# Optimization experiments

Measured on AMD Instinct MI355X. Metric: run time of the kernel, lower is better.

## Reference

```python
import jax, jax.numpy as jnp
import numpy as np

R = 3            # window radius -> (2R+1)^2 = 49 neighbors
N = 128          # grid side, n
K = 131          # 3 + 64 + 64 channels
C = 21           # num_classes
B = 2            # batch
W = (2 * R + 1) ** 2


def setup_inputs() -> dict:
    key = jax.random.key(0)
    k1, k2, k3, k4 = jax.random.split(key, 4)
    return {
        "intergrated": jax.random.normal(k1, (B, K, N, N), jnp.float32),
        "x2": jax.random.normal(k2, (B, C, N * N), jnp.float32),
        "sel_mask": jax.random.randint(k3, (B, N, N), 0, 2).astype(jnp.int32),
        "conv_parameter": jax.random.uniform(k4, (K,), jnp.float32),
    }


def _shifts(x, r):
    """Gather (2r+1)^2 shifted copies: x [..., n, n] -> [..., n, n, W].
    Entry w=(di,dj) holds x[i+di-r, j+dj-r] (zero-padded out of bounds)."""
    n = x.shape[-1]
    pad = [(0, 0)] * (x.ndim - 2) + [(r, r), (r, r)]
    xp = jnp.pad(x, pad)
    cols = [xp[..., di:di + n, dj:dj + n]
            for di in range(2 * r + 1) for dj in range(2 * r + 1)]
    return jnp.stack(cols, axis=-1)


def _rwn_single(feats, x2b, maskb, conv_parameter):
    """feats [K,n,n], x2b [C,n^2], maskb [n,n] int -> y [n^2, C]."""
    n = feats.shape[-1]
    m = maskb.astype(feats.dtype)            # sampled-pixel indicator
    xm = feats * m                            # sparse-sampled features [K,n,n]
    nbr = _shifts(xm, R)                      # [K,n,n,W] neighbor values
    valid = _shifts(jnp.ones((n, n), feats.dtype), R) > 0  # [n,n,W] in-bounds
    # per-channel windowed L1 distance, exp, per-pixel normalization (softmax
    # of +distance over the valid window, as in the original code)
    d = jnp.abs(xm[..., None] - nbr)          # [K,n,n,W]
    e = jnp.where(valid[None], jnp.exp(d), 0.0)
    a = e / e.sum(axis=-1, keepdims=True)     # rows sum to 1 per channel
    # W = sum_k conv_parameter[k] * a_k, rows only for selected pixels
    A = jnp.einsum('k,kijw->ijw', conv_parameter, a) * m[..., None]  # [n,n,W]
    # y[q,c] = sum_p W[p,q] * x2[p,c]  (W^T @ x2^T, per original col/row swap)
    feat = x2b.reshape(C, n, n)
    msg = A[None] * feat[..., None]           # [C,n,n,W]
    ypad = jnp.zeros((C, n + 2 * R, n + 2 * R), feats.dtype)
    w = 0
    for di in range(2 * R + 1):
        for dj in range(2 * R + 1):
            ypad = ypad.at[:, di:di + n, dj:dj + n].add(msg[..., w])
            w += 1
    y = ypad[:, R:R + n, R:R + n].reshape(C, n * n)
    return y.T                                 # [n^2, C]


def reference(intergrated, x2, sel_mask, conv_parameter):
    f = lambda fe, xb, mb: _rwn_single(fe, xb, mb, conv_parameter)
    return jax.vmap(f)(intergrated, x2, sel_mask)  # [B, n^2, C]
```

## Files before the change

### kernel.cpp

```cpp
#include <hip/hip_runtime.h>
#include <hip/hip_fp16.h>

#define R_ 3
#define D_ 7
#define W_ 49
#define N_ 128
#define K_ 131
#define C_ 21
#define B_ 2
#define NN (N_ * N_)
#define TI_ 8
#define TJ_ 16
#define PROWS (TI_ + 2 * R_)
#define PCOLS (TJ_ + 2 * R_)
#define PSTR 24
#define NELEM (PROWS * PCOLS)
#define LDSP (PROWS * PSTR + 8)
#define KC 8
#define KCHUNK ((K_ + KC - 1) / KC)

typedef __fp16 h2 __attribute__((ext_vector_type(2)));

__global__ __launch_bounds__(256) void rwn_affinity(
    const float* __restrict__ feats,
    const int*   __restrict__ mask,
    const float* __restrict__ cp,
    float* __restrict__ Aout)
{
    __shared__ float2 patch2[LDSP];

    const int tile = blockIdx.x;
    const int kc   = blockIdx.y;
    const int b    = blockIdx.z;
    const int tr = tile >> 3, tc = tile & 7;
    const int ti0 = tr * TI_, tj0 = tc * TJ_;

    const int tid = threadIdx.x;
    const int pix = tid >> 1;
    const int h   = tid & 1;
    const int ti = pix >> 4;
    const int tj = pix & 15;
    const int gi = ti0 + ti, gj = tj0 + tj;

    const float LOG2E = 1.4426950408889634f;
    int   soff[2];
    float swt[2];
    float ozw[2];
    int   slds[2];
    #pragma unroll
    for (int r = 0; r < 2; ++r) {
        int e = tid + r * 256;
        bool act = (e < NELEM);
        int pr = e / PCOLS, pc = e - pr * PCOLS;
        int mi = ti0 + pr - R_, mj = tj0 + pc - R_;
        bool inb = act && mi >= 0 && mi < N_ && mj >= 0 && mj < N_;
        int cmi = mi < 0 ? 0 : (mi > N_ - 1 ? N_ - 1 : mi);
        int cmj = mj < 0 ? 0 : (mj > N_ - 1 ? N_ - 1 : mj);
        soff[r] = cmi * N_ + cmj;
        swt[r]  = inb ? ((float)mask[b * NN + soff[r]] * LOG2E) : 0.f;
        ozw[r]  = inb ? 1.f : 0.f;
        slds[r] = act ? (pr * PSTR + pc) : (PROWS * PSTR + 4);
    }

    const float ph = h ? 0.f : 1.f;
    const int cbase = ti * PSTR + tj;
    const int bh = cbase + h;

    h2 Aacc[14];
    #pragma unroll
    for (int i = 0; i < 14; ++i) Aacc[i] = (h2){(__fp16)0.f, (__fp16)0.f};

    const int k0 = kc * KCHUNK;
    const int k1 = (k0 + KCHUNK < K_) ? (k0 + KCHUNK) : K_;
    const float* fb = feats + (size_t)b * K_ * NN;

    for (int e = tid; e < LDSP; e += 256) patch2[e] = make_float2(0.f, 0.f);

    const float* fk0 = fb + (size_t)k0 * NN;
    float pre0 = fk0[soff[0]] * swt[0];
    float pre1 = fk0[soff[1]] * swt[1];

    __syncthreads();

    for (int k = k0; k < k1; ++k) {
        patch2[slds[0]] = make_float2(ozw[0] * exp2f(pre0), ozw[0] * exp2f(-pre0));
        patch2[slds[1]] = make_float2(ozw[1] * exp2f(pre1), ozw[1] * exp2f(-pre1));
        float n0 = 0.f, n1 = 0.f;
        if (k + 1 < k1) {
            const float* fn = fb + (size_t)(k + 1) * NN;
            n0 = fn[soff[0]] * swt[0];
            n1 = fn[soff[1]] * swt[1];
        }
        __syncthreads();

        const float2 cpair = patch2[cbase + R_ * PSTR + R_];
        h2 ex[14];
        float dsum = 0.f;
        #pragma unroll
        for (int u = 0; u < D_; ++u) {
            #pragma unroll
            for (int m = 0; m < 2; ++m) {
                const float2 np0 = patch2[bh + u * PSTR + 4 * m];
                const float2 np1 = patch2[bh + u * PSTR + 4 * m + 2];
                float t0 = fmaxf(cpair.x * np0.y, np0.x * cpair.y);
                float t1 = fmaxf(cpair.x * np1.y, np1.x * cpair.y);
                if (m == 1) t1 *= ph;
                dsum += t0;
                dsum += t1;
                ex[u * 2 + m] = __builtin_amdgcn_cvt_pkrtz(t0, t1);
            }
        }
        const float denom = dsum + __shfl_xor(dsum, 1, 64);
        const float scale = cp[k] * __frcp_rn(denom);
        const h2 s2 = __builtin_amdgcn_cvt_pkrtz(scale, scale);
        #pragma unroll
        for (int m = 0; m < 14; ++m) Aacc[m] = ex[m] * s2 + Aacc[m];
        __syncthreads();

        pre0 = n0; pre1 = n1;
    }

    if (mask[b * NN + gi * N_ + gj] != 0) {
        const int pixg = gi * N_ + gj;
        float* ab = Aout + (size_t)b * W_ * NN + h * NN + pixg;
        #pragma unroll
        for (int u = 0; u < D_; ++u) {
            #pragma unroll
            for (int m = 0; m < 2; ++m) {
                const h2 tv = Aacc[u * 2 + m];
                atomicAdd(ab + (u * D_ + 4 * m) * NN, (float)tv[0]);
                if (h == 0 || m < 1)
                    atomicAdd(ab + (u * D_ + 4 * m + 2) * NN, (float)tv[1]);
            }
        }
    }
}

#define RSTR 22
__global__ __launch_bounds__(512, 4) void rwn_gather(
    const float* __restrict__ Aarr,
    const float* __restrict__ x2,
    float* __restrict__ out)
{
    __shared__ float red[8 * 64 * RSTR];

    const int q0 = blockIdx.x * 64;
    const int b  = blockIdx.y;
    const int tid = threadIdx.x;
    const int qh = tid & 63;
    const int wg = tid >> 6;
    const int q = q0 + qh;
    const int i = q >> 7, j = q & (N_ - 1);

    const float* Ab = Aarr + (size_t)b * W_ * NN;
    const float* xb = x2 + (size_t)b * C_ * NN;

    float acc[C_];
    #pragma unroll
    for (int c = 0; c < C_; ++c) acc[c] = 0.f;

    if (wg < D_) {
        const int pi = i - (wg - R_);
        const int cpi = pi < 0 ? 0 : (pi > N_ - 1 ? N_ - 1 : pi);
        const float rv = (pi >= 0 && pi < N_) ? 1.f : 0.f;
        const float* Aw = Ab + (size_t)wg * D_ * NN;
        #pragma unroll
        for (int v = 0; v < D_; ++v) {
            const int pj = j - (v - R_);
            const int cpj = pj < 0 ? 0 : (pj > N_ - 1 ? N_ - 1 : pj);
            const float vv = (pj >= 0 && pj < N_) ? rv : 0.f;
            const int p = cpi * N_ + cpj;
            const float a = vv * Aw[(size_t)v * NN + p];
            #pragma unroll
            for (int c = 0; c < C_; ++c)
                acc[c] += a * xb[(size_t)c * NN + p];
        }
    }

    float* rbase = red + (wg * 64 + qh) * RSTR;
    #pragma unroll
    for (int c = 0; c < C_; ++c) rbase[c] = acc[c];
    __syncthreads();

    float* ob = out + ((size_t)b * NN + q0) * C_;
    for (int e = tid; e < 64 * C_; e += 512) {
        const int qq = e / C_, cc = e - qq * C_;
        const int a = qq * RSTR + cc;
        float s = 0.f;
        #pragma unroll
        for (int pl = 0; pl < 8; ++pl)
            s += red[pl * 64 * RSTR + a];
        ob[e] = s;
    }
}

extern "C" void kernel_launch(void* const* d_in, const int* in_sizes, int n_in,
                              void* d_out, int out_size, void* d_ws, size_t ws_size,
                              hipStream_t stream) {
    const float* feats = (const float*)d_in[0];
    const float* x2    = (const float*)d_in[1];
    const int*   mask  = (const int*)d_in[2];
    const float* cp    = (const float*)d_in[3];
    float* out = (float*)d_out;

    float* Aarr = (float*)d_ws;
    const size_t Abytes = (size_t)B_ * W_ * NN * sizeof(float);

    (void)hipMemsetAsync(Aarr, 0, Abytes, stream);

    dim3 gridA(128, KC, B_);
    rwn_affinity<<<gridA, 256, 0, stream>>>(feats, mask, cp, Aarr);

    dim3 gridG(NN / 64, B_);
    rwn_gather<<<gridG, 512, 0, stream>>>(Aarr, x2, out);
}
```

Measured before the change: 149.3 us.

## Compact selected pixels per tile and double-buffer LDS patches in affinity kernel

```diff
diff --git a/kernel.cpp b/kernel.cpp
--- a/kernel.cpp
+++ b/kernel.cpp
@@ -9,15 +9,14 @@
 #define C_ 21
 #define B_ 2
 #define NN (N_ * N_)
-#define TI_ 8
+#define TI_ 16
 #define TJ_ 16
 #define PROWS (TI_ + 2 * R_)
 #define PCOLS (TJ_ + 2 * R_)
 #define PSTR 24
 #define NELEM (PROWS * PCOLS)
 #define LDSP (PROWS * PSTR + 8)
-#define KC 8
-#define KCHUNK ((K_ + KC - 1) / KC)
+#define KC 16
 
 typedef __fp16 h2 __attribute__((ext_vector_type(2)));
 
@@ -27,7 +26,9 @@
     const float* __restrict__ cp,
     float* __restrict__ Aout)
 {
-    __shared__ float2 patch2[LDSP];
+    __shared__ float2 patch2[2][LDSP];
+    __shared__ int wsum[4];
+    __shared__ unsigned char plist[256];
 
     const int tile = blockIdx.x;
     const int kc   = blockIdx.y;
@@ -36,11 +37,7 @@
     const int ti0 = tr * TI_, tj0 = tc * TJ_;
 
     const int tid = threadIdx.x;
-    const int pix = tid >> 1;
     const int h   = tid & 1;
-    const int ti = pix >> 4;
-    const int tj = pix & 15;
-    const int gi = ti0 + ti, gj = tj0 + tj;
 
     const float LOG2E = 1.4426950408889634f;
     int   soff[2];
@@ -62,46 +59,71 @@
         slds[r] = act ? (pr * PSTR + pc) : (PROWS * PSTR + 4);
     }
 
+    const int mk = mask[b * NN + (ti0 + (tid >> 4)) * N_ + (tj0 + (tid & 15))];
+    const unsigned long long bal = __ballot(mk != 0);
+    const int lane = tid & 63, wv = tid >> 6;
+    if (lane == 0) wsum[wv] = __popcll(bal);
+
+    for (int e = tid; e < 2 * LDSP; e += 256)
+        (&patch2[0][0])[e] = make_float2(0.f, 0.f);
+
+    const int k0 = kc * 8 + (kc < 3 ? kc : 3);
+    const int k1 = k0 + 8 + (kc < 3 ? 1 : 0);
+    const float* fb = feats + (size_t)b * K_ * NN;
+    const float* fk0 = fb + (size_t)k0 * NN;
+    float pr0 = fk0[soff[0]] * swt[0];
+    float pr1 = fk0[soff[1]] * swt[1];
+
+    __syncthreads();
+
+    const int nm = wsum[0] + wsum[1] + wsum[2] + wsum[3];
+    int pb = 0;
+    if (wv > 0) pb += wsum[0];
+    if (wv > 1) pb += wsum[1];
+    if (wv > 2) pb += wsum[2];
+    if (mk) plist[pb + __popcll(bal & ((1ull << lane) - 1ull))] = (unsigned char)tid;
+
+    patch2[0][slds[0]] = make_float2(ozw[0] * exp2f(pr0), ozw[0] * exp2f(-pr0));
+    patch2[0][slds[1]] = make_float2(ozw[1] * exp2f(pr1), ozw[1] * exp2f(-pr1));
+    {
+        const float* fn = fb + (size_t)(k0 + 1) * NN;
+        pr0 = fn[soff[0]] * swt[0];
+        pr1 = fn[soff[1]] * swt[1];
+    }
+    __syncthreads();
+
+    const int slot = tid >> 1;
+    const bool act0 = slot < nm;
+    const bool act1 = slot + 128 < nm;
+    int cb0 = 0, pg0 = 0, cb1 = 0, pg1 = 0;
+    if (act0) {
+        int q = plist[slot];        int qi = q >> 4, qj = q & 15;
+        cb0 = qi * PSTR + qj;       pg0 = (ti0 + qi) * N_ + (tj0 + qj);
+    }
+    if (act1) {
+        int q = plist[slot + 128];  int qi = q >> 4, qj = q & 15;
+        cb1 = qi * PSTR + qj;       pg1 = (ti0 + qi) * N_ + (tj0 + qj);
+    }
+
     const float ph = h ? 0.f : 1.f;
-    const int cbase = ti * PSTR + tj;
-    const int bh = cbase + h;
-
-    h2 Aacc[14];
-    #pragma unroll
-    for (int i = 0; i < 14; ++i) Aacc[i] = (h2){(__fp16)0.f, (__fp16)0.f};
-
-    const int k0 = kc * KCHUNK;
-    const int k1 = (k0 + KCHUNK < K_) ? (k0 + KCHUNK) : K_;
-    const float* fb = feats + (size_t)b * K_ * NN;
-
-    for (int e = tid; e < LDSP; e += 256) patch2[e] = make_float2(0.f, 0.f);
-
-    const float* fk0 = fb + (size_t)k0 * NN;
-    float pre0 = fk0[soff[0]] * swt[0];
-    float pre1 = fk0[soff[1]] * swt[1];
-
-    __syncthreads();
-
-    for (int k = k0; k < k1; ++k) {
-        patch2[slds[0]] = make_float2(ozw[0] * exp2f(pre0), ozw[0] * exp2f(-pre0));
-        patch2[slds[1]] = make_float2(ozw[1] * exp2f(pre1), ozw[1] * exp2f(-pre1));
-        float n0 = 0.f, n1 = 0.f;
-        if (k + 1 < k1) {
-            const float* fn = fb + (size_t)(k + 1) * NN;
-            n0 = fn[soff[0]] * swt[0];
-            n1 = fn[soff[1]] * swt[1];
-        }
-        __syncthreads();
-
-        const float2 cpair = patch2[cbase + R_ * PSTR + R_];
+    h2 A0[14], A1[14];
+    #pragma unroll
+    for (int i = 0; i < 14; ++i) {
+        A0[i] = (h2){(__fp16)0.f, (__fp16)0.f};
+        A1[i] = (h2){(__fp16)0.f, (__fp16)0.f};
+    }
+
+    auto tap_slot = [&](int cb, h2* Acc, float cpk, const float2* buf) {
+        const float2 cpair = buf[cb + R_ * PSTR + R_];
+        const int bh = cb + h;
         h2 ex[14];
         float dsum = 0.f;
         #pragma unroll
         for (int u = 0; u < D_; ++u) {
             #pragma unroll
             for (int m = 0; m < 2; ++m) {
-                const float2 np0 = patch2[bh + u * PSTR + 4 * m];
-                const float2 np1 = patch2[bh + u * PSTR + 4 * m + 2];
+                const float2 np0 = buf[bh + u * PSTR + 4 * m];
+                const float2 np1 = buf[bh + u * PSTR + 4 * m + 2];
                 float t0 = fmaxf(cpair.x * np0.y, np0.x * cpair.y);
                 float t1 = fmaxf(cpair.x * np1.y, np1.x * cpair.y);
                 if (m == 1) t1 *= ph;
@@ -111,29 +133,50 @@
             }
         }
         const float denom = dsum + __shfl_xor(dsum, 1, 64);
-        const float scale = cp[k] * __frcp_rn(denom);
+        const float scale = cpk * __frcp_rn(denom);
         const h2 s2 = __builtin_amdgcn_cvt_pkrtz(scale, scale);
         #pragma unroll
-        for (int m = 0; m < 14; ++m) Aacc[m] = ex[m] * s2 + Aacc[m];
+        for (int m = 0; m < 14; ++m) Acc[m] = ex[m] * s2 + Acc[m];
+    };
+
+    int p = 0;
+    for (int k = k0; k < k1; ++k) {
+        const float cpk = cp[k];
+        const float2* buf = patch2[p];
+        const float c0 = pr0, c1 = pr1;
+        if (k + 2 < k1) {
+            const float* fn = fb + (size_t)(k + 2) * NN;
+            pr0 = fn[soff[0]] * swt[0];
+            pr1 = fn[soff[1]] * swt[1];
+        }
+
+        if (act0) tap_slot(cb0, A0, cpk, buf);
+        if (act1) tap_slot(cb1, A1, cpk, buf);
+
+        if (k + 1 < k1) {
+            float2* nb = patch2[p ^ 1];
+            nb[slds[0]] = make_float2(ozw[0] * exp2f(c0), ozw[0] * exp2f(-c0));
+            nb[slds[1]] = make_float2(ozw[1] * exp2f(c1), ozw[1] * exp2f(-c1));
+        }
         __syncthreads();
-
-        pre0 = n0; pre1 = n1;
-    }
-
-    if (mask[b * NN + gi * N_ + gj] != 0) {
-        const int pixg = gi * N_ + gj;
-        float* ab = Aout + (size_t)b * W_ * NN + h * NN + pixg;
+        p ^= 1;
+    }
+
+    auto emit = [&](int pg, const h2* Acc) {
+        float* ab = Aout + (size_t)b * W_ * NN + h * NN + pg;
         #pragma unroll
         for (int u = 0; u < D_; ++u) {
             #pragma unroll
             for (int m = 0; m < 2; ++m) {
-                const h2 tv = Aacc[u * 2 + m];
+                const h2 tv = Acc[u * 2 + m];
                 atomicAdd(ab + (u * D_ + 4 * m) * NN, (float)tv[0]);
                 if (h == 0 || m < 1)
                     atomicAdd(ab + (u * D_ + 4 * m + 2) * NN, (float)tv[1]);
             }
         }
-    }
+    };
+    if (act0) emit(pg0, A0);
+    if (act1) emit(pg1, A1);
 }
 
 #define RSTR 22
@@ -208,7 +251,7 @@
 
     (void)hipMemsetAsync(Aarr, 0, Abytes, stream);
 
-    dim3 gridA(128, KC, B_);
+    dim3 gridA(64, KC, B_);
     rwn_affinity<<<gridA, 256, 0, stream>>>(feats, mask, cp, Aarr);
 
     dim3 gridG(NN / 64, B_);
```

After: 198.3 us. +32.8%, slower.

## Double-buffer affinity LDS patch and prefetch two channels ahead

Applied to the files above, without the earlier changes.

```diff
diff --git a/kernel.cpp b/kernel.cpp
--- a/kernel.cpp
+++ b/kernel.cpp
@@ -17,17 +17,16 @@
 #define NELEM (PROWS * PCOLS)
 #define LDSP (PROWS * PSTR + 8)
 #define KC 8
-#define KCHUNK ((K_ + KC - 1) / KC)
 
 typedef __fp16 h2 __attribute__((ext_vector_type(2)));
 
-__global__ __launch_bounds__(256) void rwn_affinity(
+__global__ __launch_bounds__(256, 8) void rwn_affinity(
     const float* __restrict__ feats,
     const int*   __restrict__ mask,
     const float* __restrict__ cp,
     float* __restrict__ Aout)
 {
-    __shared__ float2 patch2[LDSP];
+    __shared__ float2 patch2[2][LDSP];
 
     const int tile = blockIdx.x;
     const int kc   = blockIdx.y;
@@ -70,54 +69,81 @@
     #pragma unroll
     for (int i = 0; i < 14; ++i) Aacc[i] = (h2){(__fp16)0.f, (__fp16)0.f};
 
-    const int k0 = kc * KCHUNK;
-    const int k1 = (k0 + KCHUNK < K_) ? (k0 + KCHUNK) : K_;
+    const int k0 = kc * 16 + (kc < 3 ? kc : 3);
+    const int k1 = k0 + 16 + (kc < 3 ? 1 : 0);
     const float* fb = feats + (size_t)b * K_ * NN;
 
-    for (int e = tid; e < LDSP; e += 256) patch2[e] = make_float2(0.f, 0.f);
+    for (int e = tid; e < 2 * LDSP; e += 256)
+        (&patch2[0][0])[e] = make_float2(0.f, 0.f);
 
     const float* fk0 = fb + (size_t)k0 * NN;
-    float pre0 = fk0[soff[0]] * swt[0];
-    float pre1 = fk0[soff[1]] * swt[1];
+    float pr0 = fk0[soff[0]] * swt[0];
+    float pr1 = fk0[soff[1]] * swt[1];
 
     __syncthreads();
 
+    patch2[0][slds[0]] = make_float2(ozw[0] * exp2f(pr0), ozw[0] * exp2f(-pr0));
+    patch2[0][slds[1]] = make_float2(ozw[1] * exp2f(pr1), ozw[1] * exp2f(-pr1));
+    {
+        const float* fn = fb + (size_t)(k0 + 1) * NN;
+        pr0 = fn[soff[0]] * swt[0];
+        pr1 = fn[soff[1]] * swt[1];
+    }
+    __syncthreads();
+
+    int p = 0;
     for (int k = k0; k < k1; ++k) {
-        patch2[slds[0]] = make_float2(ozw[0] * exp2f(pre0), ozw[0] * exp2f(-pre0));
-        patch2[slds[1]] = make_float2(ozw[1] * exp2f(pre1), ozw[1] * exp2f(-pre1));
-        float n0 = 0.f, n1 = 0.f;
-        if (k + 1 < k1) {
-            const float* fn = fb + (size_t)(k + 1) * NN;
-            n0 = fn[soff[0]] * swt[0];
-            n1 = fn[soff[1]] * swt[1];
-        }
-        __syncthreads();
-
-        const float2 cpair = patch2[cbase + R_ * PSTR + R_];
+        const float cpk = cp[k];
+        const float2* buf = patch2[p];
+        const float c0 = pr0, c1 = pr1;
+        if (k + 2 < k1) {
+            const float* fn = fb + (size_t)(k + 2) * NN;
+            pr0 = fn[soff[0]] * swt[0];
+            pr1 = fn[soff[1]] * swt[1];
+        }
+
+        const float2 cpair = buf[cbase + R_ * PSTR + R_];
         h2 ex[14];
         float dsum = 0.f;
+        float2 n0 = buf[bh];
+        float2 n1 = buf[bh + 2];
+        float2 n2 = buf[bh + 4];
+        float2 n3 = buf[bh + 6];
         #pragma unroll
         for (int u = 0; u < D_; ++u) {
-            #pragma unroll
-            for (int m = 0; m < 2; ++m) {
-                const float2 np0 = patch2[bh + u * PSTR + 4 * m];
-                const float2 np1 = patch2[bh + u * PSTR + 4 * m + 2];
-                float t0 = fmaxf(cpair.x * np0.y, np0.x * cpair.y);
-                float t1 = fmaxf(cpair.x * np1.y, np1.x * cpair.y);
-                if (m == 1) t1 *= ph;
-                dsum += t0;
-                dsum += t1;
-                ex[u * 2 + m] = __builtin_amdgcn_cvt_pkrtz(t0, t1);
+            const float2 a0 = n0, a1 = n1, a2 = n2, a3 = n3;
+            if (u < D_ - 1) {
+                const int bn = bh + (u + 1) * PSTR;
+                n0 = buf[bn];
+                n1 = buf[bn + 2];
+                n2 = buf[bn + 4];
+                n3 = buf[bn + 6];
             }
+            float t0 = fmaxf(cpair.x * a0.y, a0.x * cpair.y);
+            float t1 = fmaxf(cpair.x * a1.y, a1.x * cpair.y);
+            float t2 = fmaxf(cpair.x * a2.y, a2.x * cpair.y);
+            float t3 = fmaxf(cpair.x * a3.y, a3.x * cpair.y);
+            t3 *= ph;
+            dsum += t0;
+            dsum += t1;
+            dsum += t2;
+            dsum += t3;
+            ex[u * 2]     = __builtin_amdgcn_cvt_pkrtz(t0, t1);
+            ex[u * 2 + 1] = __builtin_amdgcn_cvt_pkrtz(t2, t3);
         }
         const float denom = dsum + __shfl_xor(dsum, 1, 64);
-        const float scale = cp[k] * __frcp_rn(denom);
+        const float scale = cpk * __frcp_rn(denom);
         const h2 s2 = __builtin_amdgcn_cvt_pkrtz(scale, scale);
         #pragma unroll
         for (int m = 0; m < 14; ++m) Aacc[m] = ex[m] * s2 + Aacc[m];
+
+        if (k + 1 < k1) {
+            float2* nb = patch2[p ^ 1];
+            nb[slds[0]] = make_float2(ozw[0] * exp2f(c0), ozw[0] * exp2f(-c0));
+            nb[slds[1]] = make_float2(ozw[1] * exp2f(c1), ozw[1] * exp2f(-c1));
+        }
         __syncthreads();
-
-        pre0 = n0; pre1 = n1;
+        p ^= 1;
     }
 
     if (mask[b * NN + gi * N_ + gj] != 0) {
```

Measured after the change: 225.5 us. +51.1%, slower.

## Stage x2 halo tile in LDS for gather and split window across 4 lanes

Applied to the files above, without the earlier changes.

```diff
diff --git a/kernel.cpp b/kernel.cpp
--- a/kernel.cpp
+++ b/kernel.cpp
@@ -18,6 +18,7 @@
 #define LDSP (PROWS * PSTR + 8)
 #define KC 8
 #define KCHUNK ((K_ + KC - 1) / KC)
+#define HCELLS (PROWS * PCOLS)
 
 typedef __fp16 h2 __attribute__((ext_vector_type(2)));
 
@@ -136,61 +137,82 @@
     }
 }
 
-#define RSTR 22
-__global__ __launch_bounds__(512, 4) void rwn_gather(
+__global__ __launch_bounds__(512) void rwn_gather(
     const float* __restrict__ Aarr,
     const float* __restrict__ x2,
     float* __restrict__ out)
 {
-    __shared__ float red[8 * 64 * RSTR];
-
-    const int q0 = blockIdx.x * 64;
-    const int b  = blockIdx.y;
+    __shared__ float x2h[C_ * HCELLS];
+
+    const int tile = blockIdx.x;
+    const int b    = blockIdx.y;
+    const int tr = tile >> 3, tc = tile & 7;
+    const int gi0 = tr * TI_, gj0 = tc * TJ_;
+
     const int tid = threadIdx.x;
-    const int qh = tid & 63;
-    const int wg = tid >> 6;
-    const int q = q0 + qh;
-    const int i = q >> 7, j = q & (N_ - 1);
-
+
+    const float* xb = x2 + (size_t)b * C_ * NN;
+    for (int e = tid; e < C_ * HCELLS; e += 512) {
+        const int c = e / HCELLS, cell = e - c * HCELLS;
+        const int pr = cell / PCOLS, pc = cell - pr * PCOLS;
+        const int mi = gi0 + pr - R_, mj = gj0 + pc - R_;
+        const bool inb = (mi >= 0 && mi < N_ && mj >= 0 && mj < N_);
+        const int cmi = mi < 0 ? 0 : (mi > N_ - 1 ? N_ - 1 : mi);
+        const int cmj = mj < 0 ? 0 : (mj > N_ - 1 ? N_ - 1 : mj);
+        x2h[e] = inb ? xb[c * NN + cmi * N_ + cmj] : 0.f;
+    }
+    __syncthreads();
+
+    const int h = tid & 3;
+    const int q = tid >> 2;
+    const int qi = q >> 4, qj = q & 15;
+    const int gi = gi0 + qi, gj = gj0 + qj;
     const float* Ab = Aarr + (size_t)b * W_ * NN;
-    const float* xb = x2 + (size_t)b * C_ * NN;
+
+    float av[13];
+    int   cells[13];
+    #pragma unroll
+    for (int idx = 0; idx < 13; ++idx) {
+        int w = h + 4 * idx;
+        const float valid = (w < W_) ? 1.f : 0.f;
+        if (w >= W_) w = W_ - 1;
+        const int u = w / D_, v = w - u * D_;
+        const int pi = gi + R_ - u, pj = gj + R_ - v;
+        const int cmi = pi < 0 ? 0 : (pi > N_ - 1 ? N_ - 1 : pi);
+        const int cmj = pj < 0 ? 0 : (pj > N_ - 1 ? N_ - 1 : pj);
+        av[idx]    = valid * Ab[(size_t)w * NN + cmi * N_ + cmj];
+        cells[idx] = (qi + 2 * R_ - u) * PCOLS + (qj + 2 * R_ - v);
+    }
 
     float acc[C_];
     #pragma unroll
     for (int c = 0; c < C_; ++c) acc[c] = 0.f;
-
-    if (wg < D_) {
-        const int pi = i - (wg - R_);
-        const int cpi = pi < 0 ? 0 : (pi > N_ - 1 ? N_ - 1 : pi);
-        const float rv = (pi >= 0 && pi < N_) ? 1.f : 0.f;
-        const float* Aw = Ab + (size_t)wg * D_ * NN;
-        #pragma unroll
-        for (int v = 0; v < D_; ++v) {
-            const int pj = j - (v - R_);
-            const int cpj = pj < 0 ? 0 : (pj > N_ - 1 ? N_ - 1 : pj);
-            const float vv = (pj >= 0 && pj < N_) ? rv : 0.f;
-            const int p = cpi * N_ + cpj;
-            const float a = vv * Aw[(size_t)v * NN + p];
-            #pragma unroll
-            for (int c = 0; c < C_; ++c)
-                acc[c] += a * xb[(size_t)c * NN + p];
-        }
-    }
-
-    float* rbase = red + (wg * 64 + qh) * RSTR;
-    #pragma unroll
-    for (int c = 0; c < C_; ++c) rbase[c] = acc[c];
-    __syncthreads();
-
-    float* ob = out + ((size_t)b * NN + q0) * C_;
-    for (int e = tid; e < 64 * C_; e += 512) {
+    #pragma unroll
+    for (int idx = 0; idx < 13; ++idx) {
+        const float a = av[idx];
+        const float* xc = x2h + cells[idx];
+        #pragma unroll
+        for (int c = 0; c < C_; ++c)
+            acc[c] += a * xc[c * HCELLS];
+    }
+
+    #pragma unroll
+    for (int c = 0; c < C_; ++c) {
+        acc[c] += __shfl_xor(acc[c], 1, 64);
+        acc[c] += __shfl_xor(acc[c], 2, 64);
+    }
+
+    __syncthreads();
+    if (h == 0) {
+        float* os = x2h + q * C_;
+        #pragma unroll
+        for (int c = 0; c < C_; ++c) os[c] = acc[c];
+    }
+    __syncthreads();
+    for (int e = tid; e < TI_ * TJ_ * C_; e += 512) {
         const int qq = e / C_, cc = e - qq * C_;
-        const int a = qq * RSTR + cc;
-        float s = 0.f;
-        #pragma unroll
-        for (int pl = 0; pl < 8; ++pl)
-            s += red[pl * 64 * RSTR + a];
-        ob[e] = s;
+        const int gq = (gi0 + (qq >> 4)) * N_ + gj0 + (qq & 15);
+        out[((size_t)b * NN + gq) * C_ + cc] = x2h[e];
     }
 }
 
@@ -211,6 +233,6 @@
     dim3 gridA(128, KC, B_);
     rwn_affinity<<<gridA, 256, 0, stream>>>(feats, mask, cp, Aarr);
 
-    dim3 gridG(NN / 64, B_);
+    dim3 gridG(128, B_);
     rwn_gather<<<gridG, 512, 0, stream>>>(Aarr, x2, out);
 }
```

Measured after the change: 145.6 us. -2.5%, faster.
